# Optimization experiments

Hardware: AMD Instinct MI355X
Metric: run time of the kernel (lower is better)

The kernel has to match this reference:

```python
import jax, jax.numpy as jnp
import numpy as np

D_MODEL = 1024
D_STATE = 16
D_CONV = 4
EXPAND = 2
D_INNER = D_MODEL * EXPAND
BATCH = 2
SEQ = 1024


def setup_inputs() -> dict:
    key = jax.random.key(0)
    ks = jax.random.split(key, 9)
    s = lambda fan: 1.0 / np.sqrt(fan)
    x = jax.random.normal(ks[0], (BATCH, SEQ, D_MODEL), jnp.float32)
    W_in = jax.random.normal(ks[1], (D_MODEL, 2 * D_INNER), jnp.float32) * s(D_MODEL)
    conv_w = jax.random.normal(ks[2], (D_INNER, 1, D_CONV), jnp.float32) * s(D_CONV)
    conv_b = jax.random.normal(ks[3], (D_INNER,), jnp.float32) * 0.01
    W_xproj = jax.random.normal(ks[4], (D_INNER, 2 * D_STATE + 1), jnp.float32) * s(D_INNER)
    W_dt = jax.random.normal(ks[5], (1, D_INNER), jnp.float32)
    dt_std = 1.0 / np.sqrt(D_INNER)
    b_dt = jax.random.uniform(ks[6], (D_INNER,), jnp.float32, minval=-dt_std, maxval=dt_std)
    A_log = jnp.log(jnp.arange(1, D_STATE + 1, dtype=jnp.float32))
    Dp = jnp.ones((D_INNER,), jnp.float32)
    W_out = jax.random.normal(ks[7], (D_INNER, D_MODEL), jnp.float32) * s(D_INNER)
    return dict(x=x, W_in=W_in, conv_w=conv_w, conv_b=conv_b, W_xproj=W_xproj,
                W_dt=W_dt, b_dt=b_dt, A_log=A_log, Dp=Dp, W_out=W_out)


def _mamba_forward(x, W_in, conv_w, conv_b, W_xproj, W_dt, b_dt, A_log, Dp, W_out):
    # input projection, split into x branch and gate z
    xz = x @ W_in                              # (B, L, 2*d_inner)
    x_in, z = jnp.split(xz, 2, axis=-1)
    # causal depthwise conv1d: left-pad d_conv-1 (equiv to torch pad=d_conv-1 + truncate to L)
    xc = jnp.transpose(x_in, (0, 2, 1))        # (B, d_inner, L)
    xc = jax.lax.conv_general_dilated(
        xc, conv_w, window_strides=(1,), padding=[(D_CONV - 1, 0)],
        feature_group_count=D_INNER, dimension_numbers=('NCH', 'OIH', 'NCH'))
    xc = xc + conv_b[None, :, None]
    xc = jax.nn.silu(jnp.transpose(xc, (0, 2, 1)))  # (B, L, d_inner)
    # selective SSM
    A = -jnp.exp(A_log)                        # (N,)
    xp = xc @ W_xproj                          # (B, L, 2N+1)
    dt_raw = xp[..., :1]                       # (B, L, 1)
    B_sel = xp[..., 1:1 + D_STATE]             # (B, L, N)
    C_sel = xp[..., 1 + D_STATE:]              # (B, L, N)
    delta = jax.nn.softplus(dt_raw @ W_dt + b_dt)       # (B, L, d_inner)
    dA = jnp.exp(delta[..., None] * A)                   # (B, L, d, N)
    dBx = (delta * xc)[..., None] * B_sel[:, :, None, :]  # (B, L, d, N)

    def step(h, inp):
        dA_t, dBx_t, C_t = inp                 # (B,d,N),(B,d,N),(B,N)
        h = dA_t * h + dBx_t
        y_t = jnp.einsum('bdn,bn->bd', h, C_t)
        return h, y_t

    h0 = jnp.zeros((x.shape[0], D_INNER, D_STATE), xc.dtype)
    _, ys = jax.lax.scan(step, h0,
                         (dA.swapaxes(0, 1), dBx.swapaxes(0, 1), C_sel.swapaxes(0, 1)))
    y = ys.swapaxes(0, 1) + Dp * xc            # (B, L, d_inner)
    y = y * jax.nn.silu(z)
    return y @ W_out                           # (B, L, d_model)


def reference(x, W_in, conv_w, conv_b, W_xproj, W_dt, b_dt, A_log, Dp, W_out):
    return _mamba_forward(x, W_in, conv_w, conv_b, W_xproj, W_dt, b_dt, A_log, Dp, W_out)
```

## Files before the change

kernel.cpp:

```cpp
#include <hip/hip_runtime.h>


#define NTOK      2048
#define NC        64
#define TC        16
#define XPP_PARTS 16

typedef unsigned short u16;
typedef short short8 __attribute__((ext_vector_type(8)));
typedef u16 ushort8v __attribute__((ext_vector_type(8)));
typedef float f32x4 __attribute__((ext_vector_type(4)));

__device__ __forceinline__ float bf2f(u16 v) {
    union { unsigned int u; float f; } w; w.u = ((unsigned int)v) << 16; return w.f;
}
__device__ __forceinline__ u16 f2bf(float f) {
    union { float f; unsigned int u; } w; w.f = f;
    unsigned int u = w.u;
    return (u16)((u + 0x7fffu + ((u >> 16) & 1u)) >> 16);
}

__device__ __forceinline__ void gload_lds16(const u16* g, u16* l) {
    __builtin_amdgcn_global_load_lds(
        (const __attribute__((address_space(1))) void*)g,
        (__attribute__((address_space(3))) void*)l, 16, 0, 0);
}

__device__ __forceinline__ float softplus_f(float x) {
    return fmaxf(x, 0.f) + __logf(1.f + __expf(-__builtin_fabsf(x)));
}

__device__ __forceinline__ void transpose_tile(const float* __restrict__ in,
                                               u16* __restrict__ out,
                                               int R, int C, int n0, int k0,
                                               int tid) {
    __shared__ float tile[32][33];
    const int tx = tid & 31, ty = tid >> 5;
    #pragma unroll
    for (int i = 0; i < 32; i += 8)
        tile[ty + i][tx] = in[(size_t)(k0 + ty + i) * C + n0 + tx];
    __syncthreads();
    #pragma unroll
    for (int i = 0; i < 32; i += 8)
        out[(size_t)(n0 + ty + i) * R + k0 + tx] = f2bf(tile[tx][ty + i]);
}

__global__ __launch_bounds__(256)
void prep_all(const float* __restrict__ x, const float* __restrict__ W_in,
              const float* __restrict__ W_out, const float* __restrict__ W_xproj,
              u16* __restrict__ xbf, u16* __restrict__ WinT,
              u16* __restrict__ WoutT, u16* __restrict__ WxpT) {
    const int tid = threadIdx.x;
    int blk = blockIdx.x;
    if (blk < 2048) {
        int base = (blk * 256 + tid) * 4;
        float4 v = *(const float4*)(x + base);
        ushort4 o;
        o.x = f2bf(v.x); o.y = f2bf(v.y); o.z = f2bf(v.z); o.w = f2bf(v.w);
        *(ushort4*)(xbf + base) = o;
        return;
    }
    blk -= 2048;
    if (blk < 4096) {
        transpose_tile(W_in, WinT, 1024, 4096, (blk & 127) * 32, (blk >> 7) * 32, tid);
        return;
    }
    blk -= 4096;
    if (blk < 2048) {
        transpose_tile(W_out, WoutT, 2048, 1024, (blk & 31) * 32, (blk >> 5) * 32, tid);
        return;
    }
    blk -= 2048;
    {
        int gid = blk * 256 + tid;
        int k = gid & 2047;
        int n = gid >> 11;
        WxpT[(size_t)n * 2048 + k] = (n < 33) ? f2bf(W_xproj[(size_t)k * 33 + n]) : (u16)0;
    }
}

template <int OUT_MODE>
__global__ __launch_bounds__(256)
void gemm_bt(const u16* __restrict__ A, const u16* __restrict__ Bt,
             void* __restrict__ Cv, int M, int N, int K) {
    __shared__ __align__(16) u16 As[2][128 * 32];
    __shared__ __align__(16) u16 Bs[2][128 * 32];

    const unsigned nwg = gridDim.x * gridDim.y * gridDim.z;
    unsigned flat = blockIdx.x + gridDim.x * (blockIdx.y + gridDim.y * blockIdx.z);
    flat = (flat & 7u) * (nwg >> 3) + (flat >> 3);
    const int bx = flat % gridDim.x;
    const unsigned rem = flat / gridDim.x;
    const int by = rem % gridDim.y;
    const int bz = rem / gridDim.y;

    const int tid  = threadIdx.x;
    const int lane = tid & 63;
    const int w    = tid >> 6;
    const int wm   = (w >> 1) * 64;
    const int wn   = (w & 1) * 64;
    const int r    = lane & 15;
    const int q    = lane >> 4;
    const int m0   = bx * 128;
    const int n0   = by * 128;
    const int kChunk = K / gridDim.z;
    const int k0   = bz * kChunk;

    f32x4 acc[4][4];
    #pragma unroll
    for (int i = 0; i < 4; ++i)
        #pragma unroll
        for (int j = 0; j < 4; ++j)
            acc[i][j] = (f32x4){0.f, 0.f, 0.f, 0.f};

    for (int kk = k0; kk < k0 + kChunk; kk += 64) {
        __syncthreads();
        #pragma unroll
        for (int i = 0; i < 4; ++i) {
            int half = i >> 1;
            int c    = ((i & 1) << 8) + tid;
            int row  = c >> 2;
            int kc   = (c & 3) << 3;
            int wb   = (((i & 1) << 8) + (tid & 192)) * 8;
            gload_lds16(&A[(size_t)(m0 + row) * K + kk + half * 32 + kc],
                        &As[half][wb]);
            gload_lds16(&Bt[(size_t)(n0 + row) * K + kk + half * 32 + kc],
                        &Bs[half][wb]);
        }
        __syncthreads();

        #pragma unroll
        for (int half = 0; half < 2; ++half) {
            short8 af[4], bf[4];
            #pragma unroll
            for (int mt = 0; mt < 4; ++mt)
                af[mt] = *(const short8*)(&As[half][(wm + mt * 16 + r) * 32 + q * 8]);
            #pragma unroll
            for (int nt = 0; nt < 4; ++nt)
                bf[nt] = *(const short8*)(&Bs[half][(wn + nt * 16 + r) * 32 + q * 8]);

            #pragma unroll
            for (int mt = 0; mt < 4; ++mt)
                #pragma unroll
                for (int nt = 0; nt < 4; ++nt)
                    acc[mt][nt] = __builtin_amdgcn_mfma_f32_16x16x32_bf16(
                        af[mt], bf[nt], acc[mt][nt], 0, 0, 0);
        }
    }

    float* Cp = (float*)Cv + (size_t)bz * M * N;
    #pragma unroll
    for (int mt = 0; mt < 4; ++mt) {
        #pragma unroll
        for (int nt = 0; nt < 4; ++nt) {
            #pragma unroll
            for (int i = 0; i < 4; ++i) {
                int row = m0 + wm + mt * 16 + q * 4 + i;
                int col = n0 + wn + nt * 16 + r;
                float v = acc[mt][nt][i];
                size_t idx = (size_t)row * N + col;
                if (OUT_MODE == 0) Cp[idx] = v;
                else               ((u16*)Cv)[idx] = f2bf(v);
            }
        }
    }
}

__global__ __launch_bounds__(256)
void reduce_parts(const float4* __restrict__ p, float4* __restrict__ o,
                  int n4, int parts) {
    int i = blockIdx.x * 256 + threadIdx.x;
    if (i >= n4) return;
    float4 s = p[i];
    for (int z = 1; z < parts; ++z) {
        float4 v = p[(size_t)z * n4 + i];
        s.x += v.x; s.y += v.y; s.z += v.z; s.w += v.w;
    }
    o[i] = s;
}

__global__ __launch_bounds__(256)
void conv_silu(const u16* __restrict__ xz, const float* __restrict__ cw,
               const float* __restrict__ cb, u16* __restrict__ xcb) {
    const int tid = threadIdx.x;
    const int tok = blockIdx.x;
    const int b   = tok >> 10;
    const int t   = tok & 1023;
    const int d0  = tid << 3;

    const float4 cb0 = *(const float4*)(cb + d0);
    const float4 cb1 = *(const float4*)(cb + d0 + 4);

    ushort8v v[4];
    #pragma unroll
    for (int j = 0; j < 4; ++j) {
        const int tt = t - 3 + j;
        if (tt >= 0)
            v[j] = *(const ushort8v*)(xz + (size_t)(b * 1024 + tt) * 4096 + d0);
        else
            v[j] = (ushort8v){0, 0, 0, 0, 0, 0, 0, 0};
    }

    ushort8v o;
    #pragma unroll
    for (int k = 0; k < 8; ++k) {
        const float4 cwk = *(const float4*)(cw + (size_t)(d0 + k) * 4);
        float s = (k < 4) ? ((const float*)&cb0)[k] : ((const float*)&cb1)[k - 4];
        s += bf2f(v[0][k]) * cwk.x;
        s += bf2f(v[1][k]) * cwk.y;
        s += bf2f(v[2][k]) * cwk.z;
        s += bf2f(v[3][k]) * cwk.w;
        const float sl = s / (1.f + __expf(-s));
        o[k] = f2bf(sl);
    }
    *(ushort8v*)(xcb + (size_t)tok * 2048 + d0) = o;
}

__device__ __forceinline__ void pow_tree(float e1, float* dA) {
    float e2 = e1 * e1, e4 = e2 * e2, e8 = e4 * e4;
    dA[0] = e1;       dA[1] = e2;       dA[2] = e2 * e1;  dA[3] = e4;
    dA[4] = e4 * e1;  dA[5] = e4 * e2;  dA[6] = e4 * dA[2]; dA[7] = e8;
    dA[8] = e8 * e1;  dA[9] = e8 * e2;  dA[10] = e8 * dA[2]; dA[11] = e8 * e4;
    dA[12] = e8 * dA[4]; dA[13] = e8 * dA[5]; dA[14] = e8 * dA[6]; dA[15] = e8 * e8;
}

__device__ __forceinline__ void stage_xp(const float* __restrict__ xpp,
                                         float (*xps)[36], int tok0, int tid) {
    for (int e = tid; e < TC * 33; e += 256) {
        int t = (e * 993) >> 15;
        int j = e - t * 33;
        const float* pp = xpp + (size_t)(tok0 + t) * 128 + j;
        float s = 0.f;
        #pragma unroll
        for (int z = 0; z < XPP_PARTS; ++z)
            s += pp[(size_t)z * NTOK * 128];
        xps[t][j] = s;
    }
}

__global__ __launch_bounds__(256)
void scan_pass1(const u16* __restrict__ xcb, const float* __restrict__ xpp,
                const float* __restrict__ W_dt, const float* __restrict__ b_dt,
                const float* __restrict__ A_log,
                float* __restrict__ Sdl, float* __restrict__ hend) {
    const int c  = blockIdx.x;
    const int dg = blockIdx.y;
    const int b  = blockIdx.z;
    const int tid = threadIdx.x;
    const int d  = dg * 256 + tid;
    const int tok0 = b * 1024 + c * TC;

    __shared__ float xps[TC][36];
    stage_xp(xpp, xps, tok0, tid);
    __syncthreads();

    float a[16];
    bool fast = true;
    #pragma unroll
    for (int n = 0; n < 16; ++n) {
        a[n] = -__expf(A_log[n]);
        fast = fast && (__builtin_fabsf(a[n] + (float)(n + 1)) < 1e-3f * (n + 1));
    }

    const float wdt = W_dt[d];
    const float bdt = b_dt[d];

    float h[16];
    #pragma unroll
    for (int n = 0; n < 16; ++n) h[n] = 0.f;
    float sdl = 0.f;

    for (int t = 0; t < TC; ++t) {
        const int tok = tok0 + t;
        const float dl = softplus_f(xps[t][0] * wdt + bdt);
        sdl += dl;
        const float xv = bf2f(xcb[(size_t)tok * 2048 + d]);
        const float wv = dl * xv;
        if (fast) {
            float dA[16];
            pow_tree(__expf(-dl), dA);
            #pragma unroll
            for (int n = 0; n < 16; ++n)
                h[n] = fmaf(dA[n], h[n], wv * xps[t][1 + n]);
        } else {
            #pragma unroll
            for (int n = 0; n < 16; ++n)
                h[n] = fmaf(__expf(dl * a[n]), h[n], wv * xps[t][1 + n]);
        }
    }

    Sdl[(size_t)(b * NC + c) * 2048 + d] = sdl;
    #pragma unroll
    for (int n = 0; n < 16; ++n)
        hend[((size_t)((b * NC + c) * 16 + n)) * 2048 + d] = h[n];
}

__global__ __launch_bounds__(256)
void scan_combine(const float* __restrict__ Sdl, const float* __restrict__ A_log,
                  const float* __restrict__ hend, float* __restrict__ hstart) {
    const int gid = blockIdx.x * 256 + threadIdx.x;
    const int d = gid & 2047;
    const int n = (gid >> 11) & 15;
    const int b = gid >> 15;
    const float an = -__expf(A_log[n]);
    float H = 0.f;
    #pragma unroll 4
    for (int c = 0; c < NC; ++c) {
        size_t cidx = (size_t)(b * NC + c);
        float s  = Sdl[cidx * 2048 + d];
        size_t idx = (cidx * 16 + n) * 2048 + d;
        float he = hend[idx];
        hstart[idx] = H;
        H = fmaf(__expf(an * s), H, he);
    }
}

__global__ __launch_bounds__(256)
void scan_pass2(const u16* __restrict__ xcb, const float* __restrict__ xpp,
                const float* __restrict__ W_dt, const float* __restrict__ b_dt,
                const float* __restrict__ A_log, const float* __restrict__ Hstart,
                const float* __restrict__ Dp, const u16* __restrict__ xz,
                u16* __restrict__ ybuf) {
    const int c  = blockIdx.x;
    const int dg = blockIdx.y;
    const int b  = blockIdx.z;
    const int tid = threadIdx.x;
    const int d  = dg * 256 + tid;
    const int tok0 = b * 1024 + c * TC;

    __shared__ float xps[TC][36];
    stage_xp(xpp, xps, tok0, tid);
    __syncthreads();

    float a[16];
    bool fast = true;
    #pragma unroll
    for (int n = 0; n < 16; ++n) {
        a[n] = -__expf(A_log[n]);
        fast = fast && (__builtin_fabsf(a[n] + (float)(n + 1)) < 1e-3f * (n + 1));
    }

    const float wdt = W_dt[d];
    const float bdt = b_dt[d];

    float h[16];
    #pragma unroll
    for (int n = 0; n < 16; ++n)
        h[n] = Hstart[((size_t)((b * NC + c) * 16 + n)) * 2048 + d];

    const float Dd = Dp[d];
    for (int t = 0; t < TC; ++t) {
        const int tok = tok0 + t;
        const float dl = softplus_f(xps[t][0] * wdt + bdt);
        const float xv = bf2f(xcb[(size_t)tok * 2048 + d]);
        const float wv = dl * xv;
        if (fast) {
            float dA[16];
            pow_tree(__expf(-dl), dA);
            #pragma unroll
            for (int n = 0; n < 16; ++n)
                h[n] = fmaf(dA[n], h[n], wv * xps[t][1 + n]);
        } else {
            #pragma unroll
            for (int n = 0; n < 16; ++n)
                h[n] = fmaf(__expf(dl * a[n]), h[n], wv * xps[t][1 + n]);
        }
        float y0 = 0.f, y1 = 0.f, y2 = 0.f, y3 = 0.f;
        #pragma unroll
        for (int n = 0; n < 16; n += 4) {
            y0 = fmaf(h[n + 0], xps[t][17 + n + 0], y0);
            y1 = fmaf(h[n + 1], xps[t][17 + n + 1], y1);
            y2 = fmaf(h[n + 2], xps[t][17 + n + 2], y2);
            y3 = fmaf(h[n + 3], xps[t][17 + n + 3], y3);
        }
        float y = (y0 + y1) + (y2 + y3);
        y = fmaf(Dd, xv, y);
        float zv = bf2f(xz[(size_t)tok * 4096 + 2048 + d]);
        float sz = zv / (1.f + __expf(-zv));
        ybuf[(size_t)tok * 2048 + d] = f2bf(y * sz);
    }
}

extern "C" void kernel_launch(void* const* d_in, const int* in_sizes, int n_in,
                              void* d_out, int out_size, void* d_ws, size_t ws_size,
                              hipStream_t stream) {
    const float* x       = (const float*)d_in[0];
    const float* W_in    = (const float*)d_in[1];
    const float* conv_w  = (const float*)d_in[2];
    const float* conv_b  = (const float*)d_in[3];
    const float* W_xproj = (const float*)d_in[4];
    const float* W_dt    = (const float*)d_in[5];
    const float* b_dt    = (const float*)d_in[6];
    const float* A_log   = (const float*)d_in[7];
    const float* Dp      = (const float*)d_in[8];
    const float* W_out   = (const float*)d_in[9];
    float* out = (float*)d_out;

    char* ws = (char*)d_ws;
    size_t off = 0;
    auto alloc = [&](size_t bytes) -> void* {
        void* p = ws + off;
        off += (bytes + 255) & ~(size_t)255;
        return p;
    };

    u16*   xbf    = (u16*)  alloc((size_t)NTOK * 1024 * 2);
    u16*   xz     = (u16*)  alloc((size_t)NTOK * 4096 * 2);
    u16*   WinT   = (u16*)  alloc((size_t)4096 * 1024 * 2);
    u16*   WoutT  = (u16*)  alloc((size_t)1024 * 2048 * 2);
    u16*   WxpT   = (u16*)  alloc((size_t)128 * 2048 * 2);
    u16*   xcb    = (u16*)  alloc((size_t)NTOK * 2048 * 2);
    float* xpp    = (float*)alloc((size_t)XPP_PARTS * NTOK * 128 * 4);
    u16*   ybuf   = (u16*)  alloc((size_t)NTOK * 2048 * 2);
    float* Sdl    = (float*)alloc((size_t)2 * NC * 2048 * 4);
    float* hend   = (float*)alloc((size_t)2 * NC * 16 * 2048 * 4);
    float* hstart = (float*)alloc((size_t)2 * NC * 16 * 2048 * 4);
    float* op     = (float*)alloc((size_t)4 * NTOK * 1024 * 4);

    const int ws_ok = (off <= ws_size);
    if (ws_ok) {
        prep_all<<<9216, 256, 0, stream>>>(x, W_in, W_out, W_xproj,
                                           xbf, WinT, WoutT, WxpT);

        gemm_bt<2><<<dim3(16, 32, 1), 256, 0, stream>>>(xbf, WinT, xz,
                                                        2048, 4096, 1024);

        conv_silu<<<dim3(NTOK), 256, 0, stream>>>(xz, conv_w, conv_b, xcb);

        gemm_bt<0><<<dim3(16, 1, XPP_PARTS), 256, 0, stream>>>(xcb, WxpT, xpp,
                                                               2048, 128, 2048);

        scan_pass1<<<dim3(NC, 8, 2), 256, 0, stream>>>(xcb, xpp, W_dt, b_dt, A_log,
                                                       Sdl, hend);
        scan_combine<<<(2 * 16 * 2048) / 256, 256, 0, stream>>>(Sdl, A_log,
                                                                hend, hstart);
        scan_pass2<<<dim3(NC, 8, 2), 256, 0, stream>>>(xcb, xpp, W_dt, b_dt, A_log,
                                                       hstart, Dp, xz, ybuf);

        gemm_bt<0><<<dim3(16, 8, 4), 256, 0, stream>>>(ybuf, WoutT, op,
                                                       2048, 1024, 2048);
        reduce_parts<<<(NTOK * 1024 / 4) / 256, 256, 0, stream>>>(
            (const float4*)op, (float4*)out, NTOK * 1024 / 4, 4);
    }
}
```

Measured before the change: 214.2 us.

## Fuse causal conv+SiLU into x-projection GEMM prologue and vectorize scan combine

Removes the standalone conv_silu kernel by computing the depthwise causal conv and SiLU in the x-projection GEMM's A-tile load. The result goes into LDS for the MFMA and is also written to xcb for the scan passes. The plain LDS stores replace the async global-to-LDS load for A, and each workgroup now does its own conv work, with only 256 workgroups in the grid. Separately, scan_combine handles four channels per thread with float4 loads and stores, using a quarter of the threads.

```diff
diff --git a/kernel.cpp b/kernel.cpp
--- a/kernel.cpp
+++ b/kernel.cpp
@@ -167,6 +167,113 @@
 }
 
 __global__ __launch_bounds__(256)
+void xproj_conv(const u16* __restrict__ xz, const float* __restrict__ cw,
+                const float* __restrict__ cb, const u16* __restrict__ WxpT,
+                u16* __restrict__ xcb, float* __restrict__ xpp) {
+    __shared__ __align__(16) u16 As[2][128 * 32];
+    __shared__ __align__(16) u16 Bs[2][128 * 32];
+
+    const unsigned nwg = gridDim.x * gridDim.z;
+    unsigned flat = blockIdx.x + gridDim.x * blockIdx.z;
+    flat = (flat & 7u) * (nwg >> 3) + (flat >> 3);
+    const int bx = flat % gridDim.x;
+    const int bz = flat / gridDim.x;
+
+    const int tid  = threadIdx.x;
+    const int lane = tid & 63;
+    const int w    = tid >> 6;
+    const int wm   = (w >> 1) * 64;
+    const int wn   = (w & 1) * 64;
+    const int r    = lane & 15;
+    const int q    = lane >> 4;
+    const int m0   = bx * 128;
+    const int k0   = bz * 128;
+
+    f32x4 acc[4][4];
+    #pragma unroll
+    for (int i = 0; i < 4; ++i)
+        #pragma unroll
+        for (int j = 0; j < 4; ++j)
+            acc[i][j] = (f32x4){0.f, 0.f, 0.f, 0.f};
+
+    for (int kk = k0; kk < k0 + 128; kk += 64) {
+        __syncthreads();
+        #pragma unroll
+        for (int i = 0; i < 4; ++i) {
+            const int half = i >> 1;
+            const int c    = ((i & 1) << 8) + tid;
+            const int row  = c >> 2;
+            const int kc   = (c & 3) << 3;
+            const int wb   = (((i & 1) << 8) + (tid & 192)) * 8;
+            gload_lds16(&WxpT[(size_t)row * 2048 + kk + half * 32 + kc],
+                        &Bs[half][wb]);
+            const int tok = m0 + row;
+            const int b   = tok >> 10;
+            const int t   = tok & 1023;
+            const int d0  = kk + half * 32 + kc;
+
+            const float4 cb0 = *(const float4*)(cb + d0);
+            const float4 cb1 = *(const float4*)(cb + d0 + 4);
+            ushort8v v[4];
+            #pragma unroll
+            for (int j = 0; j < 4; ++j) {
+                const int tt = t - 3 + j;
+                v[j] = (ushort8v){0, 0, 0, 0, 0, 0, 0, 0};
+                if (tt >= 0)
+                    v[j] = *(const ushort8v*)(xz + (size_t)(b * 1024 + tt) * 4096 + d0);
+            }
+            ushort8v o;
+            #pragma unroll
+            for (int k = 0; k < 8; ++k) {
+                const float4 cwk = *(const float4*)(cw + (size_t)(d0 + k) * 4);
+                float s = (k < 4) ? ((const float*)&cb0)[k] : ((const float*)&cb1)[k - 4];
+                s += bf2f(v[0][k]) * cwk.x;
+                s += bf2f(v[1][k]) * cwk.y;
+                s += bf2f(v[2][k]) * cwk.z;
+                s += bf2f(v[3][k]) * cwk.w;
+                const float sl = s / (1.f + __expf(-s));
+                o[k] = f2bf(sl);
+            }
+            *(ushort8v*)(&As[half][(size_t)c * 8]) = o;
+            *(ushort8v*)(xcb + (size_t)tok * 2048 + d0) = o;
+        }
+        __syncthreads();
+
+        #pragma unroll
+        for (int half = 0; half < 2; ++half) {
+            short8 af[4], bf[4];
+            #pragma unroll
+            for (int mt = 0; mt < 4; ++mt)
+                af[mt] = *(const short8*)(&As[half][(wm + mt * 16 + r) * 32 + q * 8]);
+            #pragma unroll
+            for (int nt = 0; nt < 4; ++nt)
+                bf[nt] = *(const short8*)(&Bs[half][(wn + nt * 16 + r) * 32 + q * 8]);
+
+            #pragma unroll
+            for (int mt = 0; mt < 4; ++mt)
+                #pragma unroll
+                for (int nt = 0; nt < 4; ++nt)
+                    acc[mt][nt] = __builtin_amdgcn_mfma_f32_16x16x32_bf16(
+                        af[mt], bf[nt], acc[mt][nt], 0, 0, 0);
+        }
+    }
+
+    float* Cp = xpp + (size_t)bz * NTOK * 128;
+    #pragma unroll
+    for (int mt = 0; mt < 4; ++mt) {
+        #pragma unroll
+        for (int nt = 0; nt < 4; ++nt) {
+            #pragma unroll
+            for (int i = 0; i < 4; ++i) {
+                int row = m0 + wm + mt * 16 + q * 4 + i;
+                int col = wn + nt * 16 + r;
+                Cp[(size_t)row * 128 + col] = acc[mt][nt][i];
+            }
+        }
+    }
+}
+
+__global__ __launch_bounds__(256)
 void reduce_parts(const float4* __restrict__ p, float4* __restrict__ o,
                   int n4, int parts) {
     int i = blockIdx.x * 256 + threadIdx.x;
@@ -177,43 +284,6 @@
         s.x += v.x; s.y += v.y; s.z += v.z; s.w += v.w;
     }
     o[i] = s;
-}
-
-__global__ __launch_bounds__(256)
-void conv_silu(const u16* __restrict__ xz, const float* __restrict__ cw,
-               const float* __restrict__ cb, u16* __restrict__ xcb) {
-    const int tid = threadIdx.x;
-    const int tok = blockIdx.x;
-    const int b   = tok >> 10;
-    const int t   = tok & 1023;
-    const int d0  = tid << 3;
-
-    const float4 cb0 = *(const float4*)(cb + d0);
-    const float4 cb1 = *(const float4*)(cb + d0 + 4);
-
-    ushort8v v[4];
-    #pragma unroll
-    for (int j = 0; j < 4; ++j) {
-        const int tt = t - 3 + j;
-        if (tt >= 0)
-            v[j] = *(const ushort8v*)(xz + (size_t)(b * 1024 + tt) * 4096 + d0);
-        else
-            v[j] = (ushort8v){0, 0, 0, 0, 0, 0, 0, 0};
-    }
-
-    ushort8v o;
-    #pragma unroll
-    for (int k = 0; k < 8; ++k) {
-        const float4 cwk = *(const float4*)(cw + (size_t)(d0 + k) * 4);
-        float s = (k < 4) ? ((const float*)&cb0)[k] : ((const float*)&cb1)[k - 4];
-        s += bf2f(v[0][k]) * cwk.x;
-        s += bf2f(v[1][k]) * cwk.y;
-        s += bf2f(v[2][k]) * cwk.z;
-        s += bf2f(v[3][k]) * cwk.w;
-        const float sl = s / (1.f + __expf(-s));
-        o[k] = f2bf(sl);
-    }
-    *(ushort8v*)(xcb + (size_t)tok * 2048 + d0) = o;
 }
 
 __device__ __forceinline__ void pow_tree(float e1, float* dA) {
@@ -299,19 +369,22 @@
 void scan_combine(const float* __restrict__ Sdl, const float* __restrict__ A_log,
                   const float* __restrict__ hend, float* __restrict__ hstart) {
     const int gid = blockIdx.x * 256 + threadIdx.x;
-    const int d = gid & 2047;
-    const int n = (gid >> 11) & 15;
-    const int b = gid >> 15;
+    const int d4 = gid & 511;
+    const int n  = (gid >> 9) & 15;
+    const int b  = gid >> 13;
     const float an = -__expf(A_log[n]);
-    float H = 0.f;
+    float4 H = make_float4(0.f, 0.f, 0.f, 0.f);
     #pragma unroll 4
     for (int c = 0; c < NC; ++c) {
         size_t cidx = (size_t)(b * NC + c);
-        float s  = Sdl[cidx * 2048 + d];
-        size_t idx = (cidx * 16 + n) * 2048 + d;
-        float he = hend[idx];
-        hstart[idx] = H;
-        H = fmaf(__expf(an * s), H, he);
+        float4 s  = ((const float4*)Sdl)[cidx * 512 + d4];
+        size_t idx = (cidx * 16 + n) * 512 + d4;
+        float4 he = ((const float4*)hend)[idx];
+        ((float4*)hstart)[idx] = H;
+        H.x = fmaf(__expf(an * s.x), H.x, he.x);
+        H.y = fmaf(__expf(an * s.y), H.y, he.y);
+        H.z = fmaf(__expf(an * s.z), H.z, he.z);
+        H.w = fmaf(__expf(an * s.w), H.w, he.w);
     }
 }
 
@@ -425,15 +498,12 @@
         gemm_bt<2><<<dim3(16, 32, 1), 256, 0, stream>>>(xbf, WinT, xz,
                                                         2048, 4096, 1024);
 
-        conv_silu<<<dim3(NTOK), 256, 0, stream>>>(xz, conv_w, conv_b, xcb);
-
-        gemm_bt<0><<<dim3(16, 1, XPP_PARTS), 256, 0, stream>>>(xcb, WxpT, xpp,
-                                                               2048, 128, 2048);
+        xproj_conv<<<dim3(16, 1, XPP_PARTS), 256, 0, stream>>>(
+            xz, conv_w, conv_b, WxpT, xcb, xpp);
 
         scan_pass1<<<dim3(NC, 8, 2), 256, 0, stream>>>(xcb, xpp, W_dt, b_dt, A_log,
                                                        Sdl, hend);
-        scan_combine<<<(2 * 16 * 2048) / 256, 256, 0, stream>>>(Sdl, A_log,
-                                                                hend, hstart);
+        scan_combine<<<64, 256, 0, stream>>>(Sdl, A_log, hend, hstart);
         scan_pass2<<<dim3(NC, 8, 2), 256, 0, stream>>>(xcb, xpp, W_dt, b_dt, A_log,
                                                        hstart, Dp, xz, ybuf);
 
```

New measurement: 213.0 us. About the same (-0.6%).
